# Kernel optimization log

Measured on AMD Instinct MI355X. Metric: run time of the kernel, lower is better.

## Reference

```python
import jax, jax.numpy as jnp
import numpy as np

N_NODES = 100000
N_EDGES = 1600000
F_IN = 35
F_OUT = 5
K = 3
HID = 100


def setup_inputs() -> dict:
    key = jax.random.key(0)
    ks = jax.random.split(key, 20)
    p = lambda k, shape: (jax.random.normal(k, shape, dtype=jnp.float32) * 0.1)
    inp = {
        "x": jax.random.normal(ks[0], (N_NODES, F_IN), dtype=jnp.float32),
        "edge_index": jax.random.randint(ks[1], (2, N_EDGES), 0, N_NODES, dtype=jnp.int64),
        "edge_weight": jax.random.uniform(ks[2], (N_EDGES,), dtype=jnp.float32),
        # MLP warm-start: Linear(35,100) -> ReLU -> Linear(100,5)
        "W1": p(ks[3], (F_IN, HID)), "b1": p(ks[4], (HID,)),
        "W2": p(ks[5], (HID, F_OUT)), "b2": p(ks[6], (F_OUT,)),
        # DCRNN gates: DConv weights [2 directions, K, in+out, out]
        "Wz": p(ks[7], (2, K, F_IN + F_OUT, F_OUT)), "bz": p(ks[8], (F_OUT,)),
        "Wr": p(ks[9], (2, K, F_IN + F_OUT, F_OUT)), "br": p(ks[10], (F_OUT,)),
        "Wh": p(ks[11], (2, K, F_IN + F_OUT, F_OUT)), "bh": p(ks[12], (F_OUT,)),
        # head Linear(5,1)
        "Wl": p(ks[13], (F_OUT, 1)), "bl": p(ks[14], (1,)),
    }
    return inp


def reference(x, edge_index, edge_weight, W1, b1, W2, b2, Wz, bz, Wr, br, Wh, bh, Wl, bl):
    n = x.shape[0]
    src, dst = edge_index[0], edge_index[1]
    eps = jnp.asarray(1e-12, x.dtype)
    # random-walk normalization: forward (out-degree) and backward (in-degree) diffusion
    deg_out = jax.ops.segment_sum(edge_weight, src, num_segments=n)
    deg_in = jax.ops.segment_sum(edge_weight, dst, num_segments=n)
    w_fwd = edge_weight / jnp.maximum(deg_out[src], eps)  # [E]
    w_bwd = edge_weight / jnp.maximum(deg_in[dst], eps)   # [E]

    def prop_fwd(X):  # aggregate src -> dst
        return jax.ops.segment_sum(X[src] * w_fwd[:, None], dst, num_segments=n)

    def prop_bwd(X):  # aggregate dst -> src (reversed edges)
        return jax.ops.segment_sum(X[dst] * w_bwd[:, None], src, num_segments=n)

    def dconv(X, W, b):  # W: [2, K, Cin, Cout]
        k_steps = W.shape[1]
        out = X @ W[0, 0] + X @ W[1, 0]
        if k_steps > 1:
            Tf0, Tb0 = X, X
            Tf1, Tb1 = prop_fwd(X), prop_bwd(X)
            out = out + Tf1 @ W[0, 1] + Tb1 @ W[1, 1]
            for k in range(2, k_steps):
                Tf2 = 2.0 * prop_fwd(Tf1) - Tf0
                Tb2 = 2.0 * prop_bwd(Tb1) - Tb0
                out = out + Tf2 @ W[0, k] + Tb2 @ W[1, k]
                Tf0, Tf1 = Tf1, Tf2
                Tb0, Tb1 = Tb1, Tb2
        return out + b

    # MLP warm-start hidden state
    h1 = jax.nn.relu(x @ W1 + b1) @ W2 + b2  # [N, F_OUT]

    # DCRNN GRU cell
    XH = jnp.concatenate([x, h1], axis=1)           # [N, F_IN+F_OUT]
    Z = jax.nn.sigmoid(dconv(XH, Wz, bz))
    R = jax.nn.sigmoid(dconv(XH, Wr, br))
    XHr = jnp.concatenate([x, h1 * R], axis=1)
    H_tilde = jnp.tanh(dconv(XHr, Wh, bh))
    H = Z * h1 + (1.0 - Z) * H_tilde                # [N, F_OUT]

    y = jax.nn.relu(H) @ Wl + bl                    # [N, 1]
    A = w_fwd                                        # normalized adjacency weights [E]
    return y, A
```

## Files before the change

### kernel.cpp

```cpp
#include <hip/hip_runtime.h>
#include <hip/hip_fp16.h>

#define F_IN 35
#define F_OUT 5
#define HID 100
#define BSH 8
#define BMSK 255
#define MAXB 512

__device__ __forceinline__ unsigned qenc(float w) {
  unsigned b = __float_as_uint(w);
  int e = 127 - (int)((b >> 23) & 0xFF);
  unsigned m = (b >> 12) & 0x7FFu;
  if (e < 0) { e = 0; m = 0; }
  if (e > 15) { e = 15; m = 0; }
  return ((unsigned)e << 11) | m;
}
__device__ __forceinline__ float qdec(unsigned q) {
  return __uint_as_float(((127u - (q >> 11)) << 23) | ((q & 0x7FFu) << 12));
}

__device__ __forceinline__ float2 uph2(unsigned u) {
  __half2 h = *reinterpret_cast<const __half2*>(&u);
  return __half22float2(h);
}
__device__ __forceinline__ unsigned pkh2(float a, float b) {
  __half2 h = __floats2half2_rn(a, b);
  return *reinterpret_cast<const unsigned*>(&h);
}

__device__ __forceinline__ int ntli(const int* p) {
  return __builtin_nontemporal_load(p);
}
__device__ __forceinline__ float ntlf(const float* p) {
  return __builtin_nontemporal_load(p);
}
__device__ __forceinline__ void ntsf(float* p, float v) {
  __builtin_nontemporal_store(v, p);
}

__global__ __launch_bounds__(256) void prep_weights(
    const float* __restrict__ Wz, const float* __restrict__ Wr,
    const float* __restrict__ Wh,
    float* __restrict__ WpackA, float* __restrict__ WpackC) {
  int t = blockIdx.x * blockDim.x + threadIdx.x;
  if (t < 40 * 50) {
    int i = t / 50, c = t % 50;
    auto W = [&](const float* Wp, int d, int k, int o) {
      return Wp[((d * 3 + k) * 40 + i) * 5 + o];
    };
    float v;
    if (c < 5)       v = W(Wz,0,0,c)    + W(Wz,1,0,c)    - W(Wz,0,2,c)    - W(Wz,1,2,c);
    else if (c < 10) v = W(Wr,0,0,c-5)  + W(Wr,1,0,c-5)  - W(Wr,0,2,c-5)  - W(Wr,1,2,c-5);
    else if (c < 15) v = W(Wz,0,1,c-10);
    else if (c < 20) v = W(Wr,0,1,c-15);
    else if (c < 25) v = W(Wz,0,2,c-20);
    else if (c < 30) v = W(Wr,0,2,c-25);
    else if (c < 35) v = W(Wz,1,1,c-30);
    else if (c < 40) v = W(Wr,1,1,c-35);
    else if (c < 45) v = W(Wz,1,2,c-40);
    else             v = W(Wr,1,2,c-45);
    WpackA[i * 50 + c] = v;
  }
  if (t < 40 * 25) {
    int i = t / 25, c = t % 25;
    auto W = [&](const float* Wp, int d, int k, int o) {
      return Wp[((d * 3 + k) * 40 + i) * 5 + o];
    };
    float v;
    if (c < 5)       v = W(Wh,0,0,c)    + W(Wh,1,0,c)    - W(Wh,0,2,c)    - W(Wh,1,2,c);
    else if (c < 10) v = W(Wh,0,1,c-5);
    else if (c < 15) v = W(Wh,0,2,c-10);
    else if (c < 20) v = W(Wh,1,1,c-15);
    else             v = W(Wh,1,2,c-20);
    WpackC[i * 25 + c] = v;
  }
}

__global__ __launch_bounds__(256) void hist_kernel(
    const int* __restrict__ ei, int* __restrict__ bcnt_f,
    int* __restrict__ bcnt_b, int E) {
  __shared__ int h[2 * MAXB];
  for (int j = threadIdx.x; j < 2 * MAXB; j += blockDim.x) h[j] = 0;
  __syncthreads();
  for (int e = blockIdx.x * blockDim.x + threadIdx.x; e < E;
       e += gridDim.x * blockDim.x) {
    int s = ntli(ei + e), d = ntli(ei + E + e);
    atomicAdd(&h[d >> BSH], 1);
    atomicAdd(&h[MAXB + (s >> BSH)], 1);
  }
  __syncthreads();
  for (int j = threadIdx.x; j < 2 * MAXB; j += blockDim.x) {
    int v = h[j];
    if (v) {
      if (j < MAXB) atomicAdd(&bcnt_f[j], v);
      else          atomicAdd(&bcnt_b[j - MAXB], v);
    }
  }
}

__global__ __launch_bounds__(512) void scanb_kernel(
    const int* __restrict__ bcnt_f, const int* __restrict__ bcnt_b,
    int* __restrict__ bbase_f, int* __restrict__ bbase_b,
    int* __restrict__ bcur_f, int* __restrict__ bcur_b,
    int* __restrict__ rs_f, int* __restrict__ rs_b,
    int nbuck, int N, int E) {
  __shared__ int s0[MAXB], s1[MAXB];
  int t = threadIdx.x;
  s0[t] = (t < nbuck) ? bcnt_f[t] : 0;
  s1[t] = (t < nbuck) ? bcnt_b[t] : 0;
  __syncthreads();
  for (int off = 1; off < MAXB; off <<= 1) {
    int a = (t >= off) ? s0[t - off] : 0;
    int b = (t >= off) ? s1[t - off] : 0;
    __syncthreads();
    s0[t] += a; s1[t] += b;
    __syncthreads();
  }
  bbase_f[t + 1] = s0[t];
  bbase_b[t + 1] = s1[t];
  bcur_f[t] = t ? s0[t - 1] : 0;
  bcur_b[t] = t ? s1[t - 1] : 0;
  if (t == 0) { bbase_f[0] = 0; bbase_b[0] = 0; rs_f[N] = E; rs_b[N] = E; }
}

__global__ __launch_bounds__(512) void passB_kernel(
    const int* __restrict__ ei, const float* __restrict__ w,
    int* __restrict__ bcur_f, int* __restrict__ bcur_b,
    int2* __restrict__ binned_f, int2* __restrict__ binned_b, int E) {
  __shared__ int hf[MAXB], hb[MAXB], cf[MAXB], cb_[MAXB];
  int tid = threadIdx.x;
  for (int j = tid; j < MAXB; j += blockDim.x) { hf[j] = 0; hb[j] = 0; cf[j] = 0; cb_[j] = 0; }
  __syncthreads();
  size_t c0 = (size_t)blockIdx.x * E / gridDim.x;
  size_t c1 = (size_t)(blockIdx.x + 1) * E / gridDim.x;
  for (size_t e = c0 + tid; e < c1; e += blockDim.x) {
    int s = ntli(ei + e), d = ntli(ei + E + e);
    atomicAdd(&hf[d >> BSH], 1);
    atomicAdd(&hb[s >> BSH], 1);
  }
  __syncthreads();
  for (int j = tid; j < MAXB; j += blockDim.x) {
    int v = hf[j];
    if (v) hf[j] = atomicAdd(&bcur_f[j], v);
    int u = hb[j];
    if (u) hb[j] = atomicAdd(&bcur_b[j], u);
  }
  __syncthreads();
  for (size_t e = c0 + tid; e < c1; e += blockDim.x) {
    int s = ntli(ei + e), d = ntli(ei + E + e);
    int wb = __float_as_int(ntlf(w + e));
    int bf = d >> BSH;
    int pf = hf[bf] + atomicAdd(&cf[bf], 1);
    binned_f[pf] = make_int2(s | ((d & BMSK) << 17), wb);
    int bb = s >> BSH;
    int pb = hb[bb] + atomicAdd(&cb_[bb], 1);
    binned_b[pb] = make_int2(d | ((s & BMSK) << 17), wb);
  }
}

__global__ __launch_bounds__(256) void passC_kernel(
    const int2* __restrict__ binned_f, const int2* __restrict__ binned_b,
    const int* __restrict__ bbase_f, const int* __restrict__ bbase_b,
    int* __restrict__ adj_f, int* __restrict__ adj_b,
    int* __restrict__ rs_f, int* __restrict__ rs_b,
    float* __restrict__ inv_in, float* __restrict__ inv_out, int N) {
  int dir = blockIdx.y;
  const int2* binned = dir ? binned_b : binned_f;
  const int* bbase   = dir ? bbase_b  : bbase_f;
  int* adj           = dir ? adj_b    : adj_f;
  int* rs            = dir ? rs_b     : rs_f;
  float* inv         = dir ? inv_out  : inv_in;
  int b = blockIdx.x;
  int base = bbase[b], end = bbase[b + 1];
  __shared__ int cnt[256]; __shared__ float wsum[256];
  __shared__ int loc[256]; __shared__ int cur[256];
  int tid = threadIdx.x;
  cnt[tid] = 0; wsum[tid] = 0.f; cur[tid] = 0;
  __syncthreads();
  for (int i = base + tid; i < end; i += 256) {
    int2 it = binned[i];
    int nl = (it.x >> 17) & BMSK;
    atomicAdd(&cnt[nl], 1);
    atomicAdd(&wsum[nl], qdec(qenc(__int_as_float(it.y))));
  }
  __syncthreads();
  int v = cnt[tid];
  loc[tid] = v;
  __syncthreads();
  for (int off = 1; off < 256; off <<= 1) {
    int a = (tid >= off) ? loc[tid - off] : 0;
    __syncthreads();
    loc[tid] += a;
    __syncthreads();
  }
  int excl = loc[tid] - v;
  int node = (b << BSH) + tid;
  if (node < N) {
    rs[node] = base + excl;
    inv[node] = 1.f / fmaxf(wsum[tid], 1e-12f);
  }
  __syncthreads();
  loc[tid] = excl;
  __syncthreads();
  for (int i = base + tid; i < end; i += 256) {
    int2 it = binned[i];
    int nl = (it.x >> 17) & BMSK;
    int p = base + loc[nl] + atomicAdd(&cur[nl], 1);
    adj[p] = (it.x & 0x1FFFF) | (int)(qenc(__int_as_float(it.y)) << 17);
  }
}

__global__ __launch_bounds__(256) void wfout_kernel(
    const int* __restrict__ ei, const float* __restrict__ ew,
    const float* __restrict__ inv_out, float* __restrict__ wf, int E) {
  for (int e = blockIdx.x * blockDim.x + threadIdx.x; e < E;
       e += gridDim.x * blockDim.x)
    ntsf(wf + e, ntlf(ew + e) * inv_out[ntli(ei + e)]);
}

__global__ __launch_bounds__(256) void nodeA_kernel(
    const float* __restrict__ x,
    const float* __restrict__ W1, const float* __restrict__ b1,
    const float* __restrict__ W2, const float* __restrict__ b2,
    const float* __restrict__ bz, const float* __restrict__ br,
    const float* __restrict__ WpackA, const float* __restrict__ WpackC,
    const float* __restrict__ inv_out, const float* __restrict__ inv_in,
    float* __restrict__ h1, float* __restrict__ accDz,
    float* __restrict__ accDr, __half* __restrict__ PA_f,
    __half* __restrict__ PA_b, __half* __restrict__ accCx, int N) {
  __shared__ float part[4][64][5];
  int tid = threadIdx.x;
  int lane = tid & 63;
  int q = __builtin_amdgcn_readfirstlane(tid >> 6);
  int n = blockIdx.x * 64 + lane;
  bool act = n < N;
  float xv[40];
  const float* xr = x + (size_t)n * F_IN;
  #pragma unroll
  for (int i = 0; i < F_IN; i++) xv[i] = act ? xr[i] : 0.f;

  float h5[5] = {0.f, 0.f, 0.f, 0.f, 0.f};
  int hbase = q * 25;
  for (int k = 0; k < 25; k++) {
    int hh = hbase + k;
    float a = b1[hh];
    #pragma unroll
    for (int i = 0; i < F_IN; i++) a = fmaf(xv[i], W1[i * HID + hh], a);
    a = fmaxf(a, 0.f);
    #pragma unroll
    for (int o = 0; o < 5; o++) h5[o] = fmaf(a, W2[hh * 5 + o], h5[o]);
  }
  #pragma unroll
  for (int o = 0; o < 5; o++) part[q][lane][o] = h5[o];
  __syncthreads();
  #pragma unroll
  for (int o = 0; o < 5; o++) {
    h5[o] = part[0][lane][o] + part[1][lane][o] + part[2][lane][o] +
            part[3][lane][o] + b2[o];
    xv[F_IN + o] = h5[o];
  }
  if (!act) return;
  if (q == 0) {
    #pragma unroll
    for (int o = 0; o < 5; o++) h1[(size_t)n * 5 + o] = h5[o];
  }
  float sOut = inv_out[n], sIn = inv_in[n];
  int c0 = q * 19, c1 = min(c0 + 19, 75);
  for (int c = c0; c < c1; c++) {
    float a = 0.f;
    if (c < 50) {
      #pragma unroll
      for (int i = 0; i < 40; i++) a = fmaf(xv[i], WpackA[i * 50 + c], a);
    } else {
      #pragma unroll
      for (int i = 0; i < F_IN; i++) a = fmaf(xv[i], WpackC[i * 25 + (c - 50)], a);
    }
    if (c < 5)       accDz[(size_t)n * 5 + c] = a + bz[c];
    else if (c < 10) accDr[(size_t)n * 5 + (c - 5)] = a + br[c - 5];
    else if (c < 30) PA_f[(size_t)n * 20 + (c - 10)] = __float2half(a * sOut);
    else if (c < 50) PA_b[(size_t)n * 20 + (c - 30)] = __float2half(a * sIn);
    else             accCx[(size_t)n * 25 + (c - 50)] = __float2half(a);
  }
}

__global__ __launch_bounds__(256) void p1_kernel(
    const int* __restrict__ rs_f, const int* __restrict__ rs_b,
    const int* __restrict__ adj_f, const int* __restrict__ adj_b,
    const __half* __restrict__ PA_f, const __half* __restrict__ PA_b,
    const float* __restrict__ inv_out, const float* __restrict__ inv_in,
    float* __restrict__ Q1_f, float* __restrict__ Q1_b,
    __half* __restrict__ Q2_f, __half* __restrict__ Q2_b, int N) {
  int dir = blockIdx.x & 1;
  int idx = (blockIdx.x >> 1) * 256 + threadIdx.x;
  if (idx >= 2 * N) return;
  int n = idx >> 1, half = idx & 1;
  const int* rs  = dir ? rs_b : rs_f;
  const int* adj = dir ? adj_b : adj_f;
  const __half* PA = dir ? PA_b : PA_f;
  int i0 = rs[n], i1 = rs[n + 1];
  float acc[10];
  #pragma unroll
  for (int c = 0; c < 10; c++) acc[c] = 0.f;
  int i = i0;
  for (; i + 4 <= i1; i += 4) {
    int a0 = ntli(adj + i),     a1 = ntli(adj + i + 1),
        a2 = ntli(adj + i + 2), a3 = ntli(adj + i + 3);
    const unsigned* r0 = (const unsigned*)(PA + (size_t)(a0 & 0x1FFFF) * 20) + half * 5;
    const unsigned* r1 = (const unsigned*)(PA + (size_t)(a1 & 0x1FFFF) * 20) + half * 5;
    const unsigned* r2 = (const unsigned*)(PA + (size_t)(a2 & 0x1FFFF) * 20) + half * 5;
    const unsigned* r3 = (const unsigned*)(PA + (size_t)(a3 & 0x1FFFF) * 20) + half * 5;
    unsigned u0[5], u1[5], u2[5], u3[5];
    #pragma unroll
    for (int k = 0; k < 5; k++) u0[k] = r0[k];
    #pragma unroll
    for (int k = 0; k < 5; k++) u1[k] = r1[k];
    #pragma unroll
    for (int k = 0; k < 5; k++) u2[k] = r2[k];
    #pragma unroll
    for (int k = 0; k < 5; k++) u3[k] = r3[k];
    float w0 = qdec(((unsigned)a0) >> 17), w1 = qdec(((unsigned)a1) >> 17),
          w2 = qdec(((unsigned)a2) >> 17), w3 = qdec(((unsigned)a3) >> 17);
    #pragma unroll
    for (int k = 0; k < 5; k++) {
      float2 f0 = uph2(u0[k]), f1 = uph2(u1[k]), f2 = uph2(u2[k]), f3 = uph2(u3[k]);
      acc[2*k]   = fmaf(w0, f0.x, acc[2*k]);   acc[2*k+1] = fmaf(w0, f0.y, acc[2*k+1]);
      acc[2*k]   = fmaf(w1, f1.x, acc[2*k]);   acc[2*k+1] = fmaf(w1, f1.y, acc[2*k+1]);
      acc[2*k]   = fmaf(w2, f2.x, acc[2*k]);   acc[2*k+1] = fmaf(w2, f2.y, acc[2*k+1]);
      acc[2*k]   = fmaf(w3, f3.x, acc[2*k]);   acc[2*k+1] = fmaf(w3, f3.y, acc[2*k+1]);
    }
  }
  for (; i < i1; i++) {
    int a = ntli(adj + i);
    float w = qdec(((unsigned)a) >> 17);
    const unsigned* row = (const unsigned*)(PA + (size_t)(a & 0x1FFFF) * 20) + half * 5;
    #pragma unroll
    for (int k = 0; k < 5; k++) {
      float2 f = uph2(row[k]);
      acc[2*k] = fmaf(w, f.x, acc[2*k]); acc[2*k+1] = fmaf(w, f.y, acc[2*k+1]);
    }
  }
  if (!half) {
    float* q = (dir ? Q1_b : Q1_f) + (size_t)n * 10;
    #pragma unroll
    for (int c = 0; c < 10; c++) q[c] = acc[c];
  } else {
    float sc = dir ? inv_in[n] : inv_out[n];
    unsigned* q = (unsigned*)((dir ? Q2_b : Q2_f) + (size_t)n * 12);
    q[0] = pkh2(acc[0] * sc, acc[1] * sc);
    q[1] = pkh2(acc[2] * sc, acc[3] * sc);
    q[2] = pkh2(acc[4] * sc, 0.f);
    q[3] = pkh2(acc[5] * sc, acc[6] * sc);
    q[4] = pkh2(acc[7] * sc, acc[8] * sc);
    q[5] = pkh2(acc[9] * sc, 0.f);
  }
}

__global__ __launch_bounds__(256) void p2a_kernel(
    const int* __restrict__ rs_f, const int* __restrict__ rs_b,
    const int* __restrict__ adj_f, const int* __restrict__ adj_b,
    const __half* __restrict__ Q2_f, const __half* __restrict__ Q2_b,
    float* __restrict__ G_f, float* __restrict__ G_b, int N) {
  int dir = blockIdx.x & 1;
  int idx = (blockIdx.x >> 1) * 256 + threadIdx.x;
  if (idx >= 2 * N) return;
  int n = idx >> 1, grp = idx & 1;
  const int* rs  = dir ? rs_b : rs_f;
  const int* adj = dir ? adj_b : adj_f;
  const __half* Q2 = dir ? Q2_b : Q2_f;
  int i0 = rs[n], i1 = rs[n + 1];
  float a[5];
  #pragma unroll
  for (int c = 0; c < 5; c++) a[c] = 0.f;
  int i = i0;
  for (; i + 8 <= i1; i += 8) {
    int e[8];
    #pragma unroll
    for (int k = 0; k < 8; k++) e[k] = ntli(adj + i + k);
    unsigned u[8][3];
    #pragma unroll
    for (int k = 0; k < 8; k++) {
      const unsigned* row =
          (const unsigned*)(Q2 + (size_t)(e[k] & 0x1FFFF) * 12) + grp * 3;
      u[k][0] = row[0]; u[k][1] = row[1]; u[k][2] = row[2];
    }
    #pragma unroll
    for (int k = 0; k < 8; k++) {
      float w = qdec(((unsigned)e[k]) >> 17);
      float2 f0 = uph2(u[k][0]), f1 = uph2(u[k][1]), f2 = uph2(u[k][2]);
      a[0] = fmaf(w, f0.x, a[0]); a[1] = fmaf(w, f0.y, a[1]);
      a[2] = fmaf(w, f1.x, a[2]); a[3] = fmaf(w, f1.y, a[3]);
      a[4] = fmaf(w, f2.x, a[4]);
    }
  }
  for (; i < i1; i++) {
    int e = ntli(adj + i);
    float w = qdec(((unsigned)e) >> 17);
    const unsigned* row =
        (const unsigned*)(Q2 + (size_t)(e & 0x1FFFF) * 12) + grp * 3;
    float2 f0 = uph2(row[0]), f1 = uph2(row[1]), f2 = uph2(row[2]);
    a[0] = fmaf(w, f0.x, a[0]); a[1] = fmaf(w, f0.y, a[1]);
    a[2] = fmaf(w, f1.x, a[2]); a[3] = fmaf(w, f1.y, a[3]);
    a[4] = fmaf(w, f2.x, a[4]);
  }
  float* g = (dir ? G_b : G_f) + (size_t)n * 10 + grp * 5;
  #pragma unroll
  for (int c = 0; c < 5; c++) g[c] = a[c];
}

__global__ __launch_bounds__(256) void p2b_kernel(
    const float* __restrict__ G_f, const float* __restrict__ G_b,
    const float* __restrict__ Q1_f, const float* __restrict__ Q1_b,
    const float* __restrict__ accDz, const float* __restrict__ accDr,
    const __half* __restrict__ accCx, const float* __restrict__ h1,
    const float* __restrict__ bh, const float* __restrict__ WpackC,
    const float* __restrict__ inv_out, const float* __restrict__ inv_in,
    float* __restrict__ Zg, float* __restrict__ accDh,
    __half* __restrict__ PH_f, __half* __restrict__ PH_b, int N) {
  int t = blockIdx.x * blockDim.x + threadIdx.x;
  int n = t >> 1, l = t & 1;
  if (n >= N) return;
  float r[5], zv[5];
  #pragma unroll
  for (int o = 0; o < 5; o++) {
    float zA = G_f[(size_t)n * 10 + o] + G_b[(size_t)n * 10 + o];
    float rA = G_f[(size_t)n * 10 + 5 + o] + G_b[(size_t)n * 10 + 5 + o];
    float zp = accDz[(size_t)n * 5 + o] + Q1_f[(size_t)n * 10 + o] +
               Q1_b[(size_t)n * 10 + o] + 2.f * zA;
    float rp = accDr[(size_t)n * 5 + o] + Q1_f[(size_t)n * 10 + 5 + o] +
               Q1_b[(size_t)n * 10 + 5 + o] + 2.f * rA;
    zv[o] = 1.f / (1.f + __expf(-zp));
    r[o]  = 1.f / (1.f + __expf(-rp));
  }
  if (l == 0) {
    #pragma unroll
    for (int o = 0; o < 5; o++) Zg[(size_t)n * 5 + o] = zv[o];
  }
  float hr[5];
  #pragma unroll
  for (int o = 0; o < 5; o++) hr[o] = h1[(size_t)n * 5 + o] * r[o];

  float sOut = inv_out[n], sIn = inv_in[n];
  int c0 = l ? 13 : 0, c1 = l ? 25 : 13;
  for (int c = c0; c < c1; c++) {
    float acc = __half2float(accCx[(size_t)n * 25 + c]);
    #pragma unroll
    for (int o = 0; o < 5; o++) acc = fmaf(hr[o], WpackC[(F_IN + o) * 25 + c], acc);
    if (c < 5)       accDh[(size_t)n * 5 + c] = acc + bh[c];
    else if (c < 10) PH_f[(size_t)n * 12 + (c - 5)] = __float2half(acc * sOut);
    else if (c < 15) PH_f[(size_t)n * 12 + 6 + (c - 10)] = __float2half(acc * sOut);
    else if (c < 20) PH_b[(size_t)n * 12 + (c - 15)] = __float2half(acc * sIn);
    else             PH_b[(size_t)n * 12 + 6 + (c - 20)] = __float2half(acc * sIn);
  }
}

__global__ __launch_bounds__(256) void p3_kernel(
    const int* __restrict__ rs_f, const int* __restrict__ rs_b,
    const int* __restrict__ adj_f, const int* __restrict__ adj_b,
    const __half* __restrict__ PH_f, const __half* __restrict__ PH_b,
    const float* __restrict__ inv_out, const float* __restrict__ inv_in,
    float* __restrict__ Q1h_f, float* __restrict__ Q1h_b,
    __half* __restrict__ Q2h_f, __half* __restrict__ Q2h_b, int N) {
  int dir = blockIdx.x & 1;
  int idx = (blockIdx.x >> 1) * 256 + threadIdx.x;
  if (idx >= 2 * N) return;
  int n = idx >> 1, half = idx & 1;
  const int* rs  = dir ? rs_b : rs_f;
  const int* adj = dir ? adj_b : adj_f;
  const __half* PH = dir ? PH_b : PH_f;
  int i0 = rs[n], i1 = rs[n + 1];
  float acc[5];
  #pragma unroll
  for (int c = 0; c < 5; c++) acc[c] = 0.f;
  int i = i0;
  for (; i + 8 <= i1; i += 8) {
    int e[8];
    #pragma unroll
    for (int k = 0; k < 8; k++) e[k] = ntli(adj + i + k);
    unsigned u[8][3];
    #pragma unroll
    for (int k = 0; k < 8; k++) {
      const unsigned* row =
          (const unsigned*)(PH + (size_t)(e[k] & 0x1FFFF) * 12) + half * 3;
      u[k][0] = row[0]; u[k][1] = row[1]; u[k][2] = row[2];
    }
    #pragma unroll
    for (int k = 0; k < 8; k++) {
      float w = qdec(((unsigned)e[k]) >> 17);
      float2 f0 = uph2(u[k][0]), f1 = uph2(u[k][1]), f2 = uph2(u[k][2]);
      acc[0] = fmaf(w, f0.x, acc[0]); acc[1] = fmaf(w, f0.y, acc[1]);
      acc[2] = fmaf(w, f1.x, acc[2]); acc[3] = fmaf(w, f1.y, acc[3]);
      acc[4] = fmaf(w, f2.x, acc[4]);
    }
  }
  for (; i < i1; i++) {
    int a = ntli(adj + i);
    float w = qdec(((unsigned)a) >> 17);
    const unsigned* row =
        (const unsigned*)(PH + (size_t)(a & 0x1FFFF) * 12) + half * 3;
    float2 f0 = uph2(row[0]), f1 = uph2(row[1]), f2 = uph2(row[2]);
    acc[0] = fmaf(w, f0.x, acc[0]); acc[1] = fmaf(w, f0.y, acc[1]);
    acc[2] = fmaf(w, f1.x, acc[2]); acc[3] = fmaf(w, f1.y, acc[3]);
    acc[4] = fmaf(w, f2.x, acc[4]);
  }
  if (!half) {
    float* q = (dir ? Q1h_b : Q1h_f) + (size_t)n * 5;
    #pragma unroll
    for (int c = 0; c < 5; c++) q[c] = acc[c];
  } else {
    float sc = dir ? inv_in[n] : inv_out[n];
    unsigned* q = (unsigned*)((dir ? Q2h_b : Q2h_f) + (size_t)n * 8);
    q[0] = pkh2(acc[0] * sc, acc[1] * sc);
    q[1] = pkh2(acc[2] * sc, acc[3] * sc);
    q[2] = pkh2(acc[4] * sc, 0.f);
  }
}

__global__ __launch_bounds__(256) void p4_kernel(
    const int* __restrict__ rs_f, const int* __restrict__ rs_b,
    const int* __restrict__ adj_f, const int* __restrict__ adj_b,
    const __half* __restrict__ Q2h_f, const __half* __restrict__ Q2h_b,
    const float* __restrict__ Q1h_f, const float* __restrict__ Q1h_b,
    const float* __restrict__ accDh, const float* __restrict__ Zg,
    const float* __restrict__ h1, const float* __restrict__ Wl,
    const float* __restrict__ bl, float* __restrict__ y, int N) {
  int t = blockIdx.x * blockDim.x + threadIdx.x;
  int n = t >> 1, l = t & 1;
  if (n >= N) return;
  const int* rs  = l ? rs_b : rs_f;
  const int* adj = l ? adj_b : adj_f;
  const __half* Q2h = l ? Q2h_b : Q2h_f;
  float a[5];
  #pragma unroll
  for (int c = 0; c < 5; c++) a[c] = 0.f;
  int i0 = rs[n], i1 = rs[n + 1];
  int i = i0;
  for (; i + 8 <= i1; i += 8) {
    int e[8];
    #pragma unroll
    for (int k = 0; k < 8; k++) e[k] = ntli(adj + i + k);
    unsigned u[8][3];
    #pragma unroll
    for (int k = 0; k < 8; k++) {
      const unsigned* row = (const unsigned*)(Q2h + (size_t)(e[k] & 0x1FFFF) * 8);
      u[k][0] = row[0]; u[k][1] = row[1]; u[k][2] = row[2];
    }
    #pragma unroll
    for (int k = 0; k < 8; k++) {
      float w = qdec(((unsigned)e[k]) >> 17);
      float2 f0 = uph2(u[k][0]), f1 = uph2(u[k][1]), f2 = uph2(u[k][2]);
      a[0] = fmaf(w, f0.x, a[0]); a[1] = fmaf(w, f0.y, a[1]);
      a[2] = fmaf(w, f1.x, a[2]); a[3] = fmaf(w, f1.y, a[3]);
      a[4] = fmaf(w, f2.x, a[4]);
    }
  }
  for (; i < i1; i++) {
    int e = ntli(adj + i);
    float w = qdec(((unsigned)e) >> 17);
    const unsigned* row = (const unsigned*)(Q2h + (size_t)(e & 0x1FFFF) * 8);
    float2 f0 = uph2(row[0]), f1 = uph2(row[1]), f2 = uph2(row[2]);
    a[0] = fmaf(w, f0.x, a[0]); a[1] = fmaf(w, f0.y, a[1]);
    a[2] = fmaf(w, f1.x, a[2]); a[3] = fmaf(w, f1.y, a[3]);
    a[4] = fmaf(w, f2.x, a[4]);
  }
  #pragma unroll
  for (int c = 0; c < 5; c++) a[c] += __shfl_xor(a[c], 1);
  if (l) return;
  float acc = bl[0];
  #pragma unroll
  for (int o = 0; o < 5; o++) {
    float pre = accDh[(size_t)n * 5 + o] + Q1h_f[(size_t)n * 5 + o] +
                Q1h_b[(size_t)n * 5 + o] + 2.f * a[o];
    float ht = tanhf(pre);
    float z = Zg[(size_t)n * 5 + o];
    float H = z * h1[(size_t)n * 5 + o] + (1.f - z) * ht;
    acc += fmaxf(H, 0.f) * Wl[o];
  }
  y[n] = acc;
}

extern "C" void kernel_launch(void* const* d_in, const int* in_sizes, int n_in,
                              void* d_out, int out_size, void* d_ws, size_t ws_size,
                              hipStream_t stream) {
  const float* x  = (const float*)d_in[0];
  const int*   ei = (const int*)d_in[1];
  const float* ew = (const float*)d_in[2];
  const float* W1 = (const float*)d_in[3];
  const float* b1 = (const float*)d_in[4];
  const float* W2 = (const float*)d_in[5];
  const float* b2 = (const float*)d_in[6];
  const float* Wz = (const float*)d_in[7];
  const float* bz = (const float*)d_in[8];
  const float* Wr = (const float*)d_in[9];
  const float* br = (const float*)d_in[10];
  const float* Wh = (const float*)d_in[11];
  const float* bh = (const float*)d_in[12];
  const float* Wl = (const float*)d_in[13];
  const float* bl = (const float*)d_in[14];

  const int N = in_sizes[0] / F_IN;
  const int E = in_sizes[2];
  const int nbuck = ((N - 1) >> BSH) + 1;

  float* out = (float*)d_out;
  float* y_out  = out;
  float* wf_out = out + N;

  float* W = (float*)d_ws;
  size_t o = 0;
  int* bcnt_f  = (int*)(W + o); o += MAXB;
  int* bcnt_b  = (int*)(W + o); o += MAXB;
  int* bbase_f = (int*)(W + o); o += MAXB + 2;
  int* bbase_b = (int*)(W + o); o += MAXB + 2;
  int* bcur_f  = (int*)(W + o); o += MAXB;
  int* bcur_b  = (int*)(W + o); o += MAXB;
  int* rs_f    = (int*)(W + o); o += (size_t)N + 1;
  int* rs_b    = (int*)(W + o); o += (size_t)N + 1;
  float* inv_out = W + o; o += N;
  float* inv_in  = W + o; o += N;
  int* adj_f   = (int*)(W + o); o += (size_t)E;
  int* adj_b   = (int*)(W + o); o += (size_t)E;
  float* h1    = W + o; o += (size_t)5 * N;
  float* accDz = W + o; o += (size_t)5 * N;
  float* accDr = W + o; o += (size_t)5 * N;
  float* accDh = W + o; o += (size_t)5 * N;
  float* Zg    = W + o; o += (size_t)5 * N;
  __half* accCx = (__half*)(W + o); o += (size_t)13 * N;
  o = (o + 1) & ~(size_t)1;
  size_t prop0 = o;
  __half* PA_f = (__half*)(W + o); o += (size_t)10 * N;
  __half* PA_b = (__half*)(W + o); o += (size_t)10 * N;
  float* Q1_f  = W + o; o += (size_t)10 * N;
  float* Q1_b  = W + o; o += (size_t)10 * N;
  __half* Q2_f = (__half*)(W + o); o += (size_t)6 * N;
  __half* Q2_b = (__half*)(W + o); o += (size_t)6 * N;
  __half* PH_f = (__half*)(W + o); o += (size_t)6 * N;
  __half* PH_b = (__half*)(W + o); o += (size_t)6 * N;
  float* Q1h_f = W + o; o += (size_t)5 * N;
  float* Q1h_b = W + o; o += (size_t)5 * N;
  o = (o + 1) & ~(size_t)1;
  __half* Q2h_f = (__half*)(W + o); o += (size_t)4 * N;
  __half* Q2h_b = (__half*)(W + o); o += (size_t)4 * N;
  float* G_f   = W + o; o += (size_t)10 * N;
  float* G_b   = W + o; o += (size_t)10 * N;
  float* WpackA = W + o; o += 2000;
  float* WpackC = W + o; o += 1000;

  int2* binned_f = (int2*)(W + prop0);
  int2* binned_b = binned_f + E;

  const int NB2 = (2 * N + 255) / 256;
  const int NBd = 2 * ((2 * N + 255) / 256);
  const int NBn = (N + 63) / 64;

  prep_weights<<<8, 256, 0, stream>>>(Wz, Wr, Wh, WpackA, WpackC);

  hipMemsetAsync(bcnt_f, 0, 2 * MAXB * sizeof(int), stream);
  hist_kernel<<<512, 256, 0, stream>>>(ei, bcnt_f, bcnt_b, E);
  scanb_kernel<<<1, MAXB, 0, stream>>>(bcnt_f, bcnt_b, bbase_f, bbase_b,
                                       bcur_f, bcur_b, rs_f, rs_b,
                                       nbuck, N, E);
  passB_kernel<<<512, 512, 0, stream>>>(ei, ew, bcur_f, bcur_b,
                                        binned_f, binned_b, E);
  passC_kernel<<<dim3(nbuck, 2), 256, 0, stream>>>(
      binned_f, binned_b, bbase_f, bbase_b, adj_f, adj_b,
      rs_f, rs_b, inv_in, inv_out, N);
  wfout_kernel<<<1024, 256, 0, stream>>>(ei, ew, inv_out, wf_out, E);

  nodeA_kernel<<<NBn, 256, 0, stream>>>(x, W1, b1, W2, b2, bz, br, WpackA,
                                        WpackC, inv_out, inv_in,
                                        h1, accDz, accDr, PA_f, PA_b,
                                        accCx, N);

  p1_kernel<<<NBd, 256, 0, stream>>>(rs_f, rs_b, adj_f, adj_b, PA_f, PA_b,
                                     inv_out, inv_in, Q1_f, Q1_b, Q2_f, Q2_b, N);
  p2a_kernel<<<NBd, 256, 0, stream>>>(rs_f, rs_b, adj_f, adj_b, Q2_f, Q2_b,
                                      G_f, G_b, N);
  p2b_kernel<<<NB2, 256, 0, stream>>>(G_f, G_b, Q1_f, Q1_b, accDz, accDr,
                                      accCx, h1, bh, WpackC, inv_out, inv_in,
                                      Zg, accDh, PH_f, PH_b, N);
  p3_kernel<<<NBd, 256, 0, stream>>>(rs_f, rs_b, adj_f, adj_b, PH_f, PH_b,
                                     inv_out, inv_in, Q1h_f, Q1h_b,
                                     Q2h_f, Q2h_b, N);
  p4_kernel<<<NB2, 256, 0, stream>>>(rs_f, rs_b, adj_f, adj_b, Q2h_f, Q2h_b,
                                     Q1h_f, Q1h_b, accDh, Zg, h1, Wl, bl,
                                     y_out, N);
}
```

Baseline: 398.7 us.

## Split binning pass by direction and store quantized weights as 16-bit

The binning kernel now runs one grid slice per direction with 1024-thread blocks instead of handling both directions in one thread. Each slice writes a packed int id array plus a 16-bit quantized weight array, replacing the 8-byte int2 records. The quantization moves from passC into passB, which shrinks scatter-write and reread traffic for the intermediate binned edges. In exchange the edge index and weight arrays are read by two grids instead of one, and there are fewer, larger blocks.

```diff
diff --git a/kernel.cpp b/kernel.cpp
--- a/kernel.cpp
+++ b/kernel.cpp
@@ -124,49 +124,56 @@
   if (t == 0) { bbase_f[0] = 0; bbase_b[0] = 0; rs_f[N] = E; rs_b[N] = E; }
 }
 
-__global__ __launch_bounds__(512) void passB_kernel(
+__global__ __launch_bounds__(1024) void passB_kernel(
     const int* __restrict__ ei, const float* __restrict__ w,
     int* __restrict__ bcur_f, int* __restrict__ bcur_b,
-    int2* __restrict__ binned_f, int2* __restrict__ binned_b, int E) {
-  __shared__ int hf[MAXB], hb[MAXB], cf[MAXB], cb_[MAXB];
+    int* __restrict__ bid_f, int* __restrict__ bid_b,
+    unsigned short* __restrict__ bq_f, unsigned short* __restrict__ bq_b,
+    int E) {
+  __shared__ int hh[MAXB], cc[MAXB];
+  int dir = blockIdx.y;
   int tid = threadIdx.x;
-  for (int j = tid; j < MAXB; j += blockDim.x) { hf[j] = 0; hb[j] = 0; cf[j] = 0; cb_[j] = 0; }
+  for (int j = tid; j < MAXB; j += blockDim.x) { hh[j] = 0; cc[j] = 0; }
   __syncthreads();
   size_t c0 = (size_t)blockIdx.x * E / gridDim.x;
   size_t c1 = (size_t)(blockIdx.x + 1) * E / gridDim.x;
+  const int* keyc = dir ? ei : ei + E;
+  const int* othc = dir ? ei + E : ei;
+  int* bcur = dir ? bcur_b : bcur_f;
+  int* bid  = dir ? bid_b  : bid_f;
+  unsigned short* bq = dir ? bq_b : bq_f;
   for (size_t e = c0 + tid; e < c1; e += blockDim.x) {
-    int s = ntli(ei + e), d = ntli(ei + E + e);
-    atomicAdd(&hf[d >> BSH], 1);
-    atomicAdd(&hb[s >> BSH], 1);
+    int key = ntli(keyc + e);
+    atomicAdd(&hh[key >> BSH], 1);
   }
   __syncthreads();
   for (int j = tid; j < MAXB; j += blockDim.x) {
-    int v = hf[j];
-    if (v) hf[j] = atomicAdd(&bcur_f[j], v);
-    int u = hb[j];
-    if (u) hb[j] = atomicAdd(&bcur_b[j], u);
+    int v = hh[j];
+    if (v) hh[j] = atomicAdd(&bcur[j], v);
   }
   __syncthreads();
   for (size_t e = c0 + tid; e < c1; e += blockDim.x) {
-    int s = ntli(ei + e), d = ntli(ei + E + e);
-    int wb = __float_as_int(ntlf(w + e));
-    int bf = d >> BSH;
-    int pf = hf[bf] + atomicAdd(&cf[bf], 1);
-    binned_f[pf] = make_int2(s | ((d & BMSK) << 17), wb);
-    int bb = s >> BSH;
-    int pb = hb[bb] + atomicAdd(&cb_[bb], 1);
-    binned_b[pb] = make_int2(d | ((s & BMSK) << 17), wb);
+    int key = ntli(keyc + e);
+    int oth = ntli(othc + e);
+    unsigned q = qenc(ntlf(w + e));
+    int b = key >> BSH;
+    int p = hh[b] + atomicAdd(&cc[b], 1);
+    bid[p] = oth | ((key & BMSK) << 17);
+    bq[p] = (unsigned short)q;
   }
 }
 
 __global__ __launch_bounds__(256) void passC_kernel(
-    const int2* __restrict__ binned_f, const int2* __restrict__ binned_b,
+    const int* __restrict__ bid_f, const int* __restrict__ bid_b,
+    const unsigned short* __restrict__ bq_f,
+    const unsigned short* __restrict__ bq_b,
     const int* __restrict__ bbase_f, const int* __restrict__ bbase_b,
     int* __restrict__ adj_f, int* __restrict__ adj_b,
     int* __restrict__ rs_f, int* __restrict__ rs_b,
     float* __restrict__ inv_in, float* __restrict__ inv_out, int N) {
   int dir = blockIdx.y;
-  const int2* binned = dir ? binned_b : binned_f;
+  const int* bid = dir ? bid_b : bid_f;
+  const unsigned short* bq = dir ? bq_b : bq_f;
   const int* bbase   = dir ? bbase_b  : bbase_f;
   int* adj           = dir ? adj_b    : adj_f;
   int* rs            = dir ? rs_b     : rs_f;
@@ -179,10 +186,10 @@
   cnt[tid] = 0; wsum[tid] = 0.f; cur[tid] = 0;
   __syncthreads();
   for (int i = base + tid; i < end; i += 256) {
-    int2 it = binned[i];
-    int nl = (it.x >> 17) & BMSK;
+    int idv = bid[i];
+    int nl = (idv >> 17) & BMSK;
     atomicAdd(&cnt[nl], 1);
-    atomicAdd(&wsum[nl], qdec(qenc(__int_as_float(it.y))));
+    atomicAdd(&wsum[nl], qdec(bq[i]));
   }
   __syncthreads();
   int v = cnt[tid];
@@ -204,10 +211,11 @@
   loc[tid] = excl;
   __syncthreads();
   for (int i = base + tid; i < end; i += 256) {
-    int2 it = binned[i];
-    int nl = (it.x >> 17) & BMSK;
+    int idv = bid[i];
+    unsigned q = bq[i];
+    int nl = (idv >> 17) & BMSK;
     int p = base + loc[nl] + atomicAdd(&cur[nl], 1);
-    adj[p] = (it.x & 0x1FFFF) | (int)(qenc(__int_as_float(it.y)) << 17);
+    adj[p] = (idv & 0x1FFFF) | (int)(q << 17);
   }
 }
 
@@ -646,8 +654,10 @@
   float* WpackA = W + o; o += 2000;
   float* WpackC = W + o; o += 1000;
 
-  int2* binned_f = (int2*)(W + prop0);
-  int2* binned_b = binned_f + E;
+  int* bid_f = (int*)(W + prop0);
+  int* bid_b = bid_f + E;
+  unsigned short* bq_f = (unsigned short*)(bid_b + E);
+  unsigned short* bq_b = bq_f + E;
 
   const int NB2 = (2 * N + 255) / 256;
   const int NBd = 2 * ((2 * N + 255) / 256);
@@ -660,10 +670,10 @@
   scanb_kernel<<<1, MAXB, 0, stream>>>(bcnt_f, bcnt_b, bbase_f, bbase_b,
                                        bcur_f, bcur_b, rs_f, rs_b,
                                        nbuck, N, E);
-  passB_kernel<<<512, 512, 0, stream>>>(ei, ew, bcur_f, bcur_b,
-                                        binned_f, binned_b, E);
+  passB_kernel<<<dim3(128, 2), 1024, 0, stream>>>(ei, ew, bcur_f, bcur_b,
+                                                  bid_f, bid_b, bq_f, bq_b, E);
   passC_kernel<<<dim3(nbuck, 2), 256, 0, stream>>>(
-      binned_f, binned_b, bbase_f, bbase_b, adj_f, adj_b,
+      bid_f, bid_b, bq_f, bq_b, bbase_f, bbase_b, adj_f, adj_b,
       rs_f, rs_b, inv_in, inv_out, N);
   wfout_kernel<<<1024, 256, 0, stream>>>(ei, ew, inv_out, wf_out, E);
 
```

After: 410.7 us. 3.0% more time.
